# Performance work log

Measured on AMD Instinct MI355X. Metric: run time of the kernel, lower is better.

Reference implementation:

```python
import jax, jax.numpy as jnp
import numpy as np

D_MODEL = 256
N_LAYER = 16
VOCAB = 24
D_INNER = 512
D_STATE = 16
D_CONV = 4
DT_RANK = 16
B = 2
L = 2048
EPS = 1e-5


def setup_inputs() -> dict:
    key = jax.random.key(0)
    ks = jax.random.split(key, 10)
    f = lambda k, shape, s=0.02: jax.random.normal(k, shape, dtype=jnp.float32) * s
    # S4D-real style A init: A_log = log(1..d_state), broadcast over channels/layers
    a_log = jnp.tile(jnp.log(jnp.arange(1, D_STATE + 1, dtype=jnp.float32)), (N_LAYER, D_INNER, 1))
    return {
        'input_ids': jax.random.randint(ks[0], (B, L), 0, VOCAB),
        'embedding': f(ks[1], (VOCAB, D_MODEL)),
        'in_proj_w': f(ks[2], (N_LAYER, 2 * D_INNER, D_MODEL)),
        'conv_w': f(ks[3], (N_LAYER, D_INNER, D_CONV), 0.1),
        'conv_b': jnp.zeros((N_LAYER, D_INNER), dtype=jnp.float32),
        'x_proj_w': f(ks[4], (N_LAYER, DT_RANK + 2 * D_STATE, D_INNER)),
        'dt_proj_w': f(ks[5], (N_LAYER, D_INNER, DT_RANK), 0.1),
        'dt_proj_b': jnp.full((N_LAYER, D_INNER), -4.6, dtype=jnp.float32),  # softplus(-4.6) ~ 0.01 = dt_init floor
        'A_log': a_log,
        'D': jnp.ones((N_LAYER, D_INNER), dtype=jnp.float32),
        'out_proj_w': f(ks[6], (N_LAYER, D_MODEL, D_INNER), 0.005),
        'norm_w': jnp.ones((N_LAYER, D_MODEL), dtype=jnp.float32),
        'norm_f_w': jnp.ones((D_MODEL,), dtype=jnp.float32),
        'lm_head_w': f(ks[7], (20, D_MODEL)),
    }


def _rmsnorm(x, w, eps=EPS):
    return x * jax.lax.rsqrt(jnp.mean(x * x, axis=-1, keepdims=True) + eps) * w


def _selective_scan(dA, dBx, C):
    # dA, dBx: (B, L, d_inner, d_state); C: (B, L, d_state)
    # h_t = dA_t * h_{t-1} + dBx_t  (parallel associative scan over L)
    def comb(left, right):
        a_l, b_l = left
        a_r, b_r = right
        return a_l * a_r, a_r * b_l + b_r
    _, hs = jax.lax.associative_scan(comb, (dA, dBx), axis=1)
    return jnp.einsum('blds,bls->bld', hs, C)


def _mamba(h, in_w, cw, cb, xw, dtw, dtb, a_log, d_skip, ow):
    # h: (B, L, d_model)
    xz = jnp.einsum('bld,ed->ble', h, in_w)            # (B, L, 2*d_inner)
    x, z = jnp.split(xz, 2, axis=-1)
    # depthwise causal conv1d over L
    xt = jnp.transpose(x, (0, 2, 1))                   # (B, d_inner, L)
    xc = jax.lax.conv_general_dilated(
        xt, cw[:, None, :], window_strides=(1,), padding=[(D_CONV - 1, 0)],
        feature_group_count=D_INNER)
    x = jax.nn.silu(jnp.transpose(xc, (0, 2, 1)) + cb)  # (B, L, d_inner)
    dbc = jnp.einsum('bld,ed->ble', x, xw)             # (B, L, dt_rank+2*d_state)
    dt, Bm, Cm = jnp.split(dbc, [DT_RANK, DT_RANK + D_STATE], axis=-1)
    dt = jax.nn.softplus(jnp.einsum('blr,dr->bld', dt, dtw) + dtb)  # (B, L, d_inner)
    A = -jnp.exp(a_log)                                # (d_inner, d_state)
    dA = jnp.exp(dt[..., None] * A)                    # (B, L, d_inner, d_state)
    dBx = dt[..., None] * Bm[:, :, None, :] * x[..., None]
    y = _selective_scan(dA, dBx, Cm) + d_skip * x
    y = y * jax.nn.silu(z)
    return jnp.einsum('bld,ed->ble', y, ow)


def reference(input_ids, embedding, in_proj_w, conv_w, conv_b, x_proj_w,
              dt_proj_w, dt_proj_b, A_log, D, out_proj_w, norm_w, norm_f_w,
              lm_head_w):
    h = embedding[input_ids]                           # (B, L, d_model)
    residual = None
    for i in range(N_LAYER):
        residual = h + residual if residual is not None else h
        hn = _rmsnorm(residual, norm_w[i])
        h = _mamba(hn, in_proj_w[i], conv_w[i], conv_b[i], x_proj_w[i],
                   dt_proj_w[i], dt_proj_b[i], A_log[i], D[i], out_proj_w[i])
    residual = h + residual
    h = _rmsnorm(residual, norm_f_w)
    return jnp.einsum('bld,vd->blv', h, lm_head_w)     # (B, L, 20)
```

## Files before the change

### kernel.cpp

```cpp
#include <hip/hip_runtime.h>
#include <hip/hip_bf16.h>

#define D_MODEL 256
#define N_LAYER 16
#define VOCAB 24
#define D_INNER 512
#define D_STATE 16
#define D_CONV 4
#define DT_RANK 16
#define BATCH 2
#define SEQ 2048
#define NTOK (BATCH*SEQ)
#define EPS 1e-5f
#define NC 128
#define CL (SEQ/NC)
#define NSC (BATCH*D_INNER*D_STATE)
#define WCVT_BLOCKS 26112

typedef __hip_bfloat16 bf16;
typedef __attribute__((ext_vector_type(8))) short short8;
typedef __attribute__((ext_vector_type(4))) float f32x4;

__device__ __forceinline__ float silu(float v) { return v / (1.f + __expf(-v)); }
__device__ __forceinline__ float bf2f(bf16 v) { return __bfloat162float(v); }
__device__ __forceinline__ float bfs2f(short s) {
    return __uint_as_float(((unsigned)(unsigned short)s) << 16);
}
__device__ __forceinline__ short bfr(float x) {
    unsigned u = __float_as_uint(x);
    return (short)((u + 0x7fffu + ((u >> 16) & 1u)) >> 16);
}

__device__ __forceinline__ float dtdot(const float* __restrict__ rv,
                                       const float* __restrict__ wdt, float bias) {
    float p0 = bias, p1 = 0.f, p2 = 0.f, p3 = 0.f;
    #pragma unroll
    for (int r = 0; r < 4; r++) {
        p0 = fmaf(rv[r*4 + 0], wdt[r*4 + 0], p0);
        p1 = fmaf(rv[r*4 + 1], wdt[r*4 + 1], p1);
        p2 = fmaf(rv[r*4 + 2], wdt[r*4 + 2], p2);
        p3 = fmaf(rv[r*4 + 3], wdt[r*4 + 3], p3);
    }
    return (p0 + p1) + (p2 + p3);
}

__global__ void k_init(const float* __restrict__ in_w, const float* __restrict__ out_w,
                       const float* __restrict__ x_w, short* __restrict__ in_wb,
                       short* __restrict__ out_wb, short* __restrict__ x_wb,
                       const int* __restrict__ ids, const float* __restrict__ emb,
                       float* __restrict__ residual, float* __restrict__ nsum) {
    __shared__ float wred[4];
    if (blockIdx.x < WCVT_BLOCKS) {
        int idx = blockIdx.x * 256 + threadIdx.x;
        if (idx < 4194304) {
            in_wb[idx] = bfr(in_w[idx]);
        } else if (idx < 4194304 + 2097152) {
            int j = idx - 4194304;
            out_wb[j] = bfr(out_w[j]);
        } else {
            int j = idx - 4194304 - 2097152;
            x_wb[j] = bfr(x_w[j]);
        }
    } else {
        int tok = blockIdx.x - WCVT_BLOCKS, c = threadIdx.x;
        float v = emb[ids[tok] * D_MODEL + c];
        residual[tok * 256 + c] = v;
        float s = v * v;
        #pragma unroll
        for (int off = 32; off >= 1; off >>= 1) s += __shfl_xor(s, off);
        if ((c & 63) == 0) wred[c >> 6] = s;
        __syncthreads();
        if (c == 0) {
            float tot = wred[0] + wred[1] + wred[2] + wred[3];
            *(float4*)(nsum + (size_t)tok * 4) = make_float4(tot, 0.f, 0.f, 0.f);
        }
    }
}

__global__ __launch_bounds__(256) void k_gemm1_mfma(const float* __restrict__ Rres,
                                                    const float* __restrict__ nsum,
                                                    const float* __restrict__ nw,
                                                    const short* __restrict__ W16,
                                                    bf16* __restrict__ xh,
                                                    bf16* __restrict__ zb) {
    __shared__ short AsL[64 * 40];
    __shared__ short WsL[128 * 40];
    const int bm = blockIdx.x * 64, bn = blockIdx.y * 128;
    const int tid = threadIdx.x;
    const int wave = tid >> 6, lane = tid & 63;
    const int wm = (wave & 1) * 32, wn = (wave >> 1) * 32;
    const int quad = lane >> 4, lr = lane & 15;
    const int srow = tid >> 2, skq = (tid & 3) * 8;
    const float4 ns = *(const float4*)(nsum + (size_t)(bm + srow) * 4);
    const float scale = rsqrtf((ns.x + ns.y + ns.z + ns.w) * (1.f / 256.f) + EPS);
    f32x4 acc[2][2][2] = {};
    for (int k0 = 0; k0 < 256; k0 += 32) {
        float av[8], wv[8];
        *(float4*)&av[0] = *(const float4*)(Rres + (size_t)(bm + srow) * 256 + k0 + skq);
        *(float4*)&av[4] = *(const float4*)(Rres + (size_t)(bm + srow) * 256 + k0 + skq + 4);
        *(float4*)&wv[0] = *(const float4*)(nw + k0 + skq);
        *(float4*)&wv[4] = *(const float4*)(nw + k0 + skq + 4);
        short8 a8;
        #pragma unroll
        for (int j = 0; j < 8; j++) a8[j] = bfr(av[j] * scale * wv[j]);
        short8 w8[2];
        w8[0] = *(const short8*)(W16 + (size_t)(bn + srow) * 256 + k0 + skq);
        w8[1] = *(const short8*)(W16 + (size_t)(bn + 64 + srow) * 256 + k0 + skq);
        __syncthreads();
        *(short8*)&AsL[srow * 40 + skq] = a8;
        *(short8*)&WsL[srow * 40 + skq] = w8[0];
        *(short8*)&WsL[(64 + srow) * 40 + skq] = w8[1];
        __syncthreads();
        short8 af[2], bf[2][2];
        #pragma unroll
        for (int i = 0; i < 2; i++)
            af[i] = *(const short8*)&AsL[(wm + i * 16 + lr) * 40 + quad * 8];
        #pragma unroll
        for (int nb = 0; nb < 2; nb++)
            #pragma unroll
            for (int i = 0; i < 2; i++)
                bf[nb][i] = *(const short8*)&WsL[(nb * 64 + wn + i * 16 + lr) * 40 + quad * 8];
        #pragma unroll
        for (int nb = 0; nb < 2; nb++)
            #pragma unroll
            for (int mi = 0; mi < 2; mi++)
                #pragma unroll
                for (int ni = 0; ni < 2; ni++)
                    acc[nb][mi][ni] = __builtin_amdgcn_mfma_f32_16x16x32_bf16(
                        af[mi], bf[nb][ni], acc[nb][mi][ni], 0, 0, 0);
    }
    #pragma unroll
    for (int nb = 0; nb < 2; nb++) {
        #pragma unroll
        for (int mi = 0; mi < 2; mi++) {
            #pragma unroll
            for (int ni = 0; ni < 2; ni++) {
                int gcol = bn + nb * 64 + wn + ni * 16 + lr;
                #pragma unroll
                for (int r = 0; r < 4; r++) {
                    int grow = bm + wm + mi * 16 + quad * 4 + r;
                    float v = acc[nb][mi][ni][r];
                    if (gcol < 512) xh[(size_t)grow * 512 + gcol] = __float2bfloat16(v);
                    else            zb[(size_t)grow * 512 + gcol - 512] = __float2bfloat16(v);
                }
            }
        }
    }
}

__global__ __launch_bounds__(256) void k_gemm2_mfma(const bf16* __restrict__ Abf,
                                                    const short* __restrict__ W16,
                                                    float* __restrict__ residual,
                                                    float* __restrict__ nsum) {
    __shared__ short AsL[64 * 40];
    __shared__ short WsL[64 * 40];
    __shared__ float rsum[64][2];
    const short* A16 = (const short*)Abf;
    const int bm = blockIdx.x * 64, bn = blockIdx.y * 64;
    const int tid = threadIdx.x;
    const int wave = tid >> 6, lane = tid & 63;
    const int wm = (wave & 1) * 32, wn = (wave >> 1) * 32;
    const int quad = lane >> 4, lr = lane & 15;
    const int srow = tid >> 2, skq = (tid & 3) * 8;
    f32x4 acc[2][2] = {};
    for (int k0 = 0; k0 < 512; k0 += 32) {
        short8 a8 = *(const short8*)(A16 + (size_t)(bm + srow) * 512 + k0 + skq);
        short8 w8 = *(const short8*)(W16 + (size_t)(bn + srow) * 512 + k0 + skq);
        __syncthreads();
        *(short8*)&AsL[srow * 40 + skq] = a8;
        *(short8*)&WsL[srow * 40 + skq] = w8;
        __syncthreads();
        short8 af[2], bf[2];
        #pragma unroll
        for (int i = 0; i < 2; i++) {
            af[i] = *(const short8*)&AsL[(wm + i * 16 + lr) * 40 + quad * 8];
            bf[i] = *(const short8*)&WsL[(wn + i * 16 + lr) * 40 + quad * 8];
        }
        #pragma unroll
        for (int mi = 0; mi < 2; mi++)
            #pragma unroll
            for (int ni = 0; ni < 2; ni++)
                acc[mi][ni] = __builtin_amdgcn_mfma_f32_16x16x32_bf16(
                    af[mi], bf[ni], acc[mi][ni], 0, 0, 0);
    }
    float sq[2][4] = {};
    #pragma unroll
    for (int mi = 0; mi < 2; mi++) {
        #pragma unroll
        for (int ni = 0; ni < 2; ni++) {
            int gcol = bn + wn + ni * 16 + lr;
            #pragma unroll
            for (int r = 0; r < 4; r++) {
                int grow = bm + wm + mi * 16 + quad * 4 + r;
                size_t idx = (size_t)grow * 256 + gcol;
                float v = residual[idx] + acc[mi][ni][r];
                residual[idx] = v;
                sq[mi][r] += v * v;
            }
        }
    }
    #pragma unroll
    for (int off = 1; off < 16; off <<= 1) {
        #pragma unroll
        for (int mi = 0; mi < 2; mi++)
            #pragma unroll
            for (int r = 0; r < 4; r++)
                sq[mi][r] += __shfl_xor(sq[mi][r], off);
    }
    if (lr == 0) {
        #pragma unroll
        for (int mi = 0; mi < 2; mi++)
            #pragma unroll
            for (int r = 0; r < 4; r++)
                rsum[wm + mi * 16 + quad * 4 + r][wave >> 1] = sq[mi][r];
    }
    __syncthreads();
    if (tid < 64)
        nsum[(size_t)(bm + tid) * 4 + blockIdx.y] = rsum[tid][0] + rsum[tid][1];
}

__global__ __launch_bounds__(256) void k_cxs(const bf16* __restrict__ xh,
                                             const float* __restrict__ cw,
                                             const float* __restrict__ cb,
                                             const short* __restrict__ W16,
                                             const float* __restrict__ dtw,
                                             const float* __restrict__ dtb,
                                             const float* __restrict__ a_log,
                                             bf16* __restrict__ xb,
                                             float* __restrict__ dbc,
                                             float* __restrict__ Aprod,
                                             float* __restrict__ Hfin) {
    __shared__ short Cs[16][520];
    __shared__ float Ds[16][52];
    const int bm = blockIdx.x * 16;
    const int tid = threadIdx.x;
    const int wave = tid >> 6, lane = tid & 63;
    const int quad = lane >> 4, lr = lane & 15;
    const int wn = wave * 16;

    short8 wreg[16];
    if (wn < 48) {
        const short* wp = W16 + (size_t)(wn + lr) * 512 + quad * 8;
        #pragma unroll
        for (int k = 0; k < 16; k++) wreg[k] = *(const short8*)(wp + k * 32);
    }

    {
        const int d8 = (tid & 63) * 8;
        const int rg = (tid >> 6) * 4;
        const int lbase = (bm & 2047) + rg;
        const int gbase = bm + rg;
        float xv[7][8];
        #pragma unroll
        for (int i = 0; i < 7; i++) {
            int l = lbase - 3 + i;
            if (l >= 0) {
                short8 r8 = *(const short8*)((const short*)xh +
                               (size_t)(gbase - 3 + i) * 512 + d8);
                #pragma unroll
                for (int j = 0; j < 8; j++) xv[i][j] = bfs2f(r8[j]);
            } else {
                #pragma unroll
                for (int j = 0; j < 8; j++) xv[i][j] = 0.f;
            }
        }
        float cwv[8][4], cbv[8];
        #pragma unroll
        for (int j = 0; j < 8; j++) {
            *(float4*)&cwv[j][0] = *(const float4*)(cw + (d8 + j) * 4);
            cbv[j] = cb[d8 + j];
        }
        #pragma unroll
        for (int t = 0; t < 4; t++) {
            short8 o;
            #pragma unroll
            for (int j = 0; j < 8; j++) {
                float acc = cbv[j] + xv[t][j] * cwv[j][0] + xv[t+1][j] * cwv[j][1]
                                   + xv[t+2][j] * cwv[j][2] + xv[t+3][j] * cwv[j][3];
                o[j] = bfr(silu(acc));
            }
            *(short8*)&Cs[rg + t][d8] = o;
            *(short8*)((short*)xb + (size_t)(gbase + t) * 512 + d8) = o;
        }
    }
    __syncthreads();

    if (wn < 48) {
        f32x4 acc = {};
        #pragma unroll
        for (int k = 0; k < 16; k++) {
            short8 af = *(const short8*)&Cs[lr][k * 32 + quad * 8];
            acc = __builtin_amdgcn_mfma_f32_16x16x32_bf16(af, wreg[k], acc, 0, 0, 0);
        }
        int gcol = wn + lr;
        #pragma unroll
        for (int r = 0; r < 4; r++) {
            float v = acc[r];
            dbc[(size_t)(bm + quad * 4 + r) * 48 + gcol] = v;
            Ds[quad * 4 + r][gcol] = v;
        }
    }
    __syncthreads();

    {
        const int b = bm >> 11;
        const int c = (bm & 2047) >> 4;
        float A[2][16], h[2][16], ap[2][16], wdt[2][16], bdt[2];
        #pragma unroll
        for (int ch = 0; ch < 2; ch++) {
            int d = tid + ch * 256;
            #pragma unroll
            for (int q = 0; q < 4; q++)
                *(float4*)&wdt[ch][q*4] = *(const float4*)(dtw + d * 16 + q * 4);
            #pragma unroll
            for (int s = 0; s < 16; s++) {
                A[ch][s] = -__expf(a_log[d * 16 + s]);
                h[ch][s] = 0.f; ap[ch][s] = 1.f;
            }
            bdt[ch] = dtb[d];
        }
        for (int t = 0; t < CL; t++) {
            float dtc[16], Bc[16];
            #pragma unroll
            for (int r = 0; r < 16; r++) dtc[r] = Ds[t][r];
            #pragma unroll
            for (int s = 0; s < 16; s++) Bc[s] = Ds[t][16 + s];
            #pragma unroll
            for (int ch = 0; ch < 2; ch++) {
                int d = tid + ch * 256;
                float dtr = dtdot(dtc, wdt[ch], bdt[ch]);
                float dtv = (dtr > 20.f) ? dtr : __logf(1.f + __expf(dtr));
                float u = dtv * bfs2f(((const short*)&Cs[t][0])[d]);
                #pragma unroll
                for (int s = 0; s < 16; s++) {
                    float dA = __expf(dtv * A[ch][s]);
                    h[ch][s] = fmaf(dA, h[ch][s], u * Bc[s]);
                    ap[ch][s] *= dA;
                }
            }
        }
        #pragma unroll
        for (int ch = 0; ch < 2; ch++) {
            int d = tid + ch * 256;
            int bd = b * 512 + d;
            float* Ap = Aprod + (size_t)c * NSC + (size_t)bd * 16;
            float* Hp = Hfin  + (size_t)c * NSC + (size_t)bd * 16;
            #pragma unroll
            for (int q = 0; q < 4; q++) {
                *(float4*)(Ap + q * 4) = make_float4(ap[ch][q*4], ap[ch][q*4+1],
                                                     ap[ch][q*4+2], ap[ch][q*4+3]);
                *(float4*)(Hp + q * 4) = make_float4(h[ch][q*4], h[ch][q*4+1],
                                                     h[ch][q*4+2], h[ch][q*4+3]);
            }
        }
    }
}

__global__ __launch_bounds__(64) void k_scanB(const float* __restrict__ Aprod,
                                              float* __restrict__ Hfin) {
    int chain = blockIdx.x * 64 + threadIdx.x;
    float h = 0.f;
    for (int cg = 0; cg < NC; cg += 16) {
        float a[16], f[16];
        #pragma unroll
        for (int j = 0; j < 16; j++) {
            size_t i = (size_t)(cg + j) * NSC + chain;
            a[j] = Aprod[i];
            f[j] = Hfin[i];
        }
        #pragma unroll
        for (int j = 0; j < 16; j++) {
            size_t i = (size_t)(cg + j) * NSC + chain;
            Hfin[i] = h;
            h = fmaf(a[j], h, f[j]);
        }
    }
}

__global__ __launch_bounds__(64) void k_scanC(const bf16* __restrict__ xb,
                                              const bf16* __restrict__ zb,
                                              const float* __restrict__ dbc,
                                              const float* __restrict__ dtw,
                                              const float* __restrict__ dtb,
                                              const float* __restrict__ a_log,
                                              const float* __restrict__ Dp,
                                              const float* __restrict__ Hstart,
                                              bf16* __restrict__ yb) {
    __shared__ float DbcS[16 * 48];
    int gid = blockIdx.x * 64 + threadIdx.x;
    int bd = gid & 1023;
    int c = gid >> 10;
    int d = bd & 511, b = bd >> 9;
    int tok0 = b * SEQ + c * CL;
    {
        const float4* src = (const float4*)(dbc + (size_t)tok0 * 48);
        float4* dst = (float4*)DbcS;
        #pragma unroll
        for (int q = 0; q < 3; q++)
            dst[q * 64 + threadIdx.x] = src[q * 64 + threadIdx.x];
    }
    float A[16], h[16], wdt[16];
    const float* Hp = Hstart + (size_t)c * NSC + bd * 16;
    #pragma unroll
    for (int q = 0; q < 4; q++)
        *(float4*)&wdt[q*4] = *(const float4*)(dtw + d * 16 + q * 4);
    #pragma unroll
    for (int s = 0; s < 16; s++) {
        A[s] = -__expf(a_log[d * 16 + s]);
        h[s] = Hp[s];
    }
    float bdt = dtb[d];
    float Dv = Dp[d];
    const bf16* xp = xb + (size_t)tok0 * 512 + d;
    const bf16* zp = zb + (size_t)tok0 * 512 + d;
    bf16* yp = yb + (size_t)tok0 * 512 + d;
    __syncthreads();
    for (int t = 0; t < CL; t++) {
        float rv[48];
        #pragma unroll
        for (int q = 0; q < 12; q++)
            *(float4*)&rv[q*4] = *(const float4*)&DbcS[t * 48 + q * 4];
        float dtr = dtdot(rv, wdt, bdt);
        float dtv = (dtr > 20.f) ? dtr : __logf(1.f + __expf(dtr));
        float xv = bf2f(xp[t * 512]);
        float u = dtv * xv;
        float sum = 0.f;
        #pragma unroll
        for (int s = 0; s < 16; s++) {
            float dA = __expf(dtv * A[s]);
            h[s] = fmaf(dA, h[s], u * rv[16 + s]);
            sum = fmaf(h[s], rv[32 + s], sum);
        }
        float zv = bf2f(zp[t * 512]);
        yp[t * 512] = __float2bfloat16((sum + Dv * xv) * silu(zv));
    }
}

__global__ void k_rmshead(const float* __restrict__ residual, const float* __restrict__ w,
                          const float* __restrict__ lw, float* __restrict__ out) {
    __shared__ float wred[4];
    __shared__ float hrow[256];
    int tok = blockIdx.x, c = threadIdx.x;
    float v = residual[tok * 256 + c];
    float s = v * v;
    #pragma unroll
    for (int off = 32; off >= 1; off >>= 1) s += __shfl_xor(s, off);
    if ((c & 63) == 0) wred[c >> 6] = s;
    __syncthreads();
    float tot = wred[0] + wred[1] + wred[2] + wred[3];
    float scale = rsqrtf(tot * (1.f / 256.f) + EPS);
    hrow[c] = bfs2f(bfr(v * scale * w[c]));
    __syncthreads();
    int wave = c >> 6, lane = c & 63;
    float4 hl = *(const float4*)&hrow[lane * 4];
    #pragma unroll
    for (int j = 0; j < 5; j++) {
        int vv = wave * 5 + j;
        float4 wl = *(const float4*)(lw + (size_t)vv * 256 + lane * 4);
        float p = hl.x * wl.x + hl.y * wl.y + hl.z * wl.z + hl.w * wl.w;
        #pragma unroll
        for (int off = 32; off >= 1; off >>= 1) p += __shfl_xor(p, off);
        if (lane == 0) out[(size_t)tok * 20 + vv] = p;
    }
}

extern "C" void kernel_launch(void* const* d_in, const int* in_sizes, int n_in,
                              void* d_out, int out_size, void* d_ws, size_t ws_size,
                              hipStream_t stream) {
    const int*   ids    = (const int*)d_in[0];
    const float* emb    = (const float*)d_in[1];
    const float* in_w   = (const float*)d_in[2];
    const float* conv_w = (const float*)d_in[3];
    const float* conv_b = (const float*)d_in[4];
    const float* x_w    = (const float*)d_in[5];
    const float* dt_w   = (const float*)d_in[6];
    const float* dt_b   = (const float*)d_in[7];
    const float* a_log  = (const float*)d_in[8];
    const float* d_skip = (const float*)d_in[9];
    const float* out_w  = (const float*)d_in[10];
    const float* norm_w = (const float*)d_in[11];
    const float* norm_f = (const float*)d_in[12];
    const float* lm_w   = (const float*)d_in[13];
    float* out = (float*)d_out;

    char* ws = (char*)d_ws;
    float* residual = (float*)(ws + 0);
    bf16*  xh       = (bf16*) (ws + 6291456);
    bf16*  zb       = (bf16*) (ws + 10485760);
    bf16*  xb       = (bf16*) (ws + 14680064);
    float* dbc      = (float*)(ws + 18874368);
    float* Aprod    = (float*)(ws + 23855104);
    float* Hfin     = (float*)(ws + 32243712);
    short* in_wb    = (short*)(ws + 40632320);
    short* out_wb   = (short*)(ws + 49020928);
    short* x_wb     = (short*)(ws + 53215232);
    float* nsum     = (float*)(ws + 54001664);
    bf16*  yb       = xh;

    k_init<<<WCVT_BLOCKS + NTOK, 256, 0, stream>>>(in_w, out_w, x_w, in_wb, out_wb,
                                                   x_wb, ids, emb, residual, nsum);

    for (int i = 0; i < N_LAYER; i++) {
        dim3 g1(NTOK / 64, 1024 / 128);
        k_gemm1_mfma<<<g1, 256, 0, stream>>>(residual, nsum, norm_w + i * D_MODEL,
                                             in_wb + (size_t)i * 262144, xh, zb);
        k_cxs<<<NTOK / 16, 256, 0, stream>>>(
            xh, conv_w + (size_t)i * 512 * 4, conv_b + (size_t)i * 512,
            x_wb + (size_t)i * 24576, dt_w + (size_t)i * 512 * 16,
            dt_b + (size_t)i * 512, a_log + (size_t)i * 512 * 16,
            xb, dbc, Aprod, Hfin);
        k_scanB<<<NSC / 64, 64, 0, stream>>>(Aprod, Hfin);
        k_scanC<<<(1024 * NC) / 64, 64, 0, stream>>>(
            xb, zb, dbc, dt_w + (size_t)i * 512 * 16, dt_b + (size_t)i * 512,
            a_log + (size_t)i * 512 * 16, d_skip + (size_t)i * 512, Hfin, yb);
        dim3 g2(NTOK / 64, 256 / 64);
        k_gemm2_mfma<<<g2, 256, 0, stream>>>(yb, out_wb + (size_t)i * 131072,
                                             residual, nsum);
    }

    k_rmshead<<<NTOK, 256, 0, stream>>>(residual, norm_f, lm_w, out);
}
```

Before: 1.124 ms.

## Fuse chunked scan output pass with out_proj GEMM and residual update

Merges the scan-output kernel and the out_proj GEMM into one kernel. Each block handles one 16-token chunk: it runs the scan for all 512 channels (two channels per thread), writes y into shared memory as bf16, then runs an MFMA GEMM against the full 256x512 out_proj weight and updates the residual and the partial RMS sums. This avoids writing y to global memory, reading it back, and one launch per layer. In exchange each block reloads the whole weight matrix, parallelism drops from 2048 blocks of 64 threads to 256 blocks of 256 threads, and the GEMM runs with only 16 rows per block.

```diff
diff --git a/kernel.cpp b/kernel.cpp
--- a/kernel.cpp
+++ b/kernel.cpp
@@ -148,77 +148,6 @@
     }
 }
 
-__global__ __launch_bounds__(256) void k_gemm2_mfma(const bf16* __restrict__ Abf,
-                                                    const short* __restrict__ W16,
-                                                    float* __restrict__ residual,
-                                                    float* __restrict__ nsum) {
-    __shared__ short AsL[64 * 40];
-    __shared__ short WsL[64 * 40];
-    __shared__ float rsum[64][2];
-    const short* A16 = (const short*)Abf;
-    const int bm = blockIdx.x * 64, bn = blockIdx.y * 64;
-    const int tid = threadIdx.x;
-    const int wave = tid >> 6, lane = tid & 63;
-    const int wm = (wave & 1) * 32, wn = (wave >> 1) * 32;
-    const int quad = lane >> 4, lr = lane & 15;
-    const int srow = tid >> 2, skq = (tid & 3) * 8;
-    f32x4 acc[2][2] = {};
-    for (int k0 = 0; k0 < 512; k0 += 32) {
-        short8 a8 = *(const short8*)(A16 + (size_t)(bm + srow) * 512 + k0 + skq);
-        short8 w8 = *(const short8*)(W16 + (size_t)(bn + srow) * 512 + k0 + skq);
-        __syncthreads();
-        *(short8*)&AsL[srow * 40 + skq] = a8;
-        *(short8*)&WsL[srow * 40 + skq] = w8;
-        __syncthreads();
-        short8 af[2], bf[2];
-        #pragma unroll
-        for (int i = 0; i < 2; i++) {
-            af[i] = *(const short8*)&AsL[(wm + i * 16 + lr) * 40 + quad * 8];
-            bf[i] = *(const short8*)&WsL[(wn + i * 16 + lr) * 40 + quad * 8];
-        }
-        #pragma unroll
-        for (int mi = 0; mi < 2; mi++)
-            #pragma unroll
-            for (int ni = 0; ni < 2; ni++)
-                acc[mi][ni] = __builtin_amdgcn_mfma_f32_16x16x32_bf16(
-                    af[mi], bf[ni], acc[mi][ni], 0, 0, 0);
-    }
-    float sq[2][4] = {};
-    #pragma unroll
-    for (int mi = 0; mi < 2; mi++) {
-        #pragma unroll
-        for (int ni = 0; ni < 2; ni++) {
-            int gcol = bn + wn + ni * 16 + lr;
-            #pragma unroll
-            for (int r = 0; r < 4; r++) {
-                int grow = bm + wm + mi * 16 + quad * 4 + r;
-                size_t idx = (size_t)grow * 256 + gcol;
-                float v = residual[idx] + acc[mi][ni][r];
-                residual[idx] = v;
-                sq[mi][r] += v * v;
-            }
-        }
-    }
-    #pragma unroll
-    for (int off = 1; off < 16; off <<= 1) {
-        #pragma unroll
-        for (int mi = 0; mi < 2; mi++)
-            #pragma unroll
-            for (int r = 0; r < 4; r++)
-                sq[mi][r] += __shfl_xor(sq[mi][r], off);
-    }
-    if (lr == 0) {
-        #pragma unroll
-        for (int mi = 0; mi < 2; mi++)
-            #pragma unroll
-            for (int r = 0; r < 4; r++)
-                rsum[wm + mi * 16 + quad * 4 + r][wave >> 1] = sq[mi][r];
-    }
-    __syncthreads();
-    if (tid < 64)
-        nsum[(size_t)(bm + tid) * 4 + blockIdx.y] = rsum[tid][0] + rsum[tid][1];
-}
-
 __global__ __launch_bounds__(256) void k_cxs(const bf16* __restrict__ xh,
                                              const float* __restrict__ cw,
                                              const float* __restrict__ cb,
@@ -377,62 +306,116 @@
     }
 }
 
-__global__ __launch_bounds__(64) void k_scanC(const bf16* __restrict__ xb,
-                                              const bf16* __restrict__ zb,
-                                              const float* __restrict__ dbc,
-                                              const float* __restrict__ dtw,
-                                              const float* __restrict__ dtb,
-                                              const float* __restrict__ a_log,
-                                              const float* __restrict__ Dp,
-                                              const float* __restrict__ Hstart,
-                                              bf16* __restrict__ yb) {
+__global__ __launch_bounds__(256) void k_sg2(const bf16* __restrict__ xb,
+                                             const bf16* __restrict__ zb,
+                                             const float* __restrict__ dbc,
+                                             const float* __restrict__ dtw,
+                                             const float* __restrict__ dtb,
+                                             const float* __restrict__ a_log,
+                                             const float* __restrict__ Dp,
+                                             const float* __restrict__ Hstart,
+                                             const short* __restrict__ W16,
+                                             float* __restrict__ residual,
+                                             float* __restrict__ nsum) {
+    __shared__ short Ys[16][520];
     __shared__ float DbcS[16 * 48];
-    int gid = blockIdx.x * 64 + threadIdx.x;
-    int bd = gid & 1023;
-    int c = gid >> 10;
-    int d = bd & 511, b = bd >> 9;
-    int tok0 = b * SEQ + c * CL;
-    {
-        const float4* src = (const float4*)(dbc + (size_t)tok0 * 48);
-        float4* dst = (float4*)DbcS;
-        #pragma unroll
-        for (int q = 0; q < 3; q++)
-            dst[q * 64 + threadIdx.x] = src[q * 64 + threadIdx.x];
-    }
-    float A[16], h[16], wdt[16];
-    const float* Hp = Hstart + (size_t)c * NSC + bd * 16;
-    #pragma unroll
-    for (int q = 0; q < 4; q++)
-        *(float4*)&wdt[q*4] = *(const float4*)(dtw + d * 16 + q * 4);
-    #pragma unroll
-    for (int s = 0; s < 16; s++) {
-        A[s] = -__expf(a_log[d * 16 + s]);
-        h[s] = Hp[s];
-    }
-    float bdt = dtb[d];
-    float Dv = Dp[d];
-    const bf16* xp = xb + (size_t)tok0 * 512 + d;
-    const bf16* zp = zb + (size_t)tok0 * 512 + d;
-    bf16* yp = yb + (size_t)tok0 * 512 + d;
+    __shared__ short Ws[256 * 40];
+    const int bm = blockIdx.x * 16;
+    const int tid = threadIdx.x;
+    const int b = bm >> 11;
+    const int c = (bm & 2047) >> 4;
+
+    if (tid < 192)
+        ((float4*)DbcS)[tid] = ((const float4*)(dbc + (size_t)bm * 48))[tid];
+
+    float A[2][16], h[2][16], wdt[2][16], bdt[2], Dv[2];
+    #pragma unroll
+    for (int ch = 0; ch < 2; ch++) {
+        int d = tid + ch * 256;
+        int bd = b * 512 + d;
+        const float* Hp = Hstart + (size_t)c * NSC + (size_t)bd * 16;
+        #pragma unroll
+        for (int q = 0; q < 4; q++)
+            *(float4*)&wdt[ch][q*4] = *(const float4*)(dtw + d * 16 + q * 4);
+        #pragma unroll
+        for (int s = 0; s < 16; s++) {
+            A[ch][s] = -__expf(a_log[d * 16 + s]);
+            h[ch][s] = Hp[s];
+        }
+        bdt[ch] = dtb[d];
+        Dv[ch] = Dp[d];
+    }
     __syncthreads();
+
     for (int t = 0; t < CL; t++) {
         float rv[48];
         #pragma unroll
         for (int q = 0; q < 12; q++)
             *(float4*)&rv[q*4] = *(const float4*)&DbcS[t * 48 + q * 4];
-        float dtr = dtdot(rv, wdt, bdt);
-        float dtv = (dtr > 20.f) ? dtr : __logf(1.f + __expf(dtr));
-        float xv = bf2f(xp[t * 512]);
-        float u = dtv * xv;
-        float sum = 0.f;
-        #pragma unroll
-        for (int s = 0; s < 16; s++) {
-            float dA = __expf(dtv * A[s]);
-            h[s] = fmaf(dA, h[s], u * rv[16 + s]);
-            sum = fmaf(h[s], rv[32 + s], sum);
-        }
-        float zv = bf2f(zp[t * 512]);
-        yp[t * 512] = __float2bfloat16((sum + Dv * xv) * silu(zv));
+        #pragma unroll
+        for (int ch = 0; ch < 2; ch++) {
+            int d = tid + ch * 256;
+            float dtr = dtdot(rv, wdt[ch], bdt[ch]);
+            float dtv = (dtr > 20.f) ? dtr : __logf(1.f + __expf(dtr));
+            float xv = bf2f(xb[(size_t)(bm + t) * 512 + d]);
+            float u = dtv * xv;
+            float sum = 0.f;
+            #pragma unroll
+            for (int s = 0; s < 16; s++) {
+                float dA = __expf(dtv * A[ch][s]);
+                h[ch][s] = fmaf(dA, h[ch][s], u * rv[16 + s]);
+                sum = fmaf(h[ch][s], rv[32 + s], sum);
+            }
+            float zv = bf2f(zb[(size_t)(bm + t) * 512 + d]);
+            Ys[t][d] = bfr((sum + Dv[ch] * xv) * silu(zv));
+        }
+    }
+    __syncthreads();
+
+    const int wave = tid >> 6, lane = tid & 63;
+    const int quad = lane >> 4, lr = lane & 15;
+    const int wn = wave * 64;
+    f32x4 acc[4] = {};
+    for (int k0 = 0; k0 < 512; k0 += 32) {
+        short8 w8[4];
+        #pragma unroll
+        for (int j = 0; j < 4; j++)
+            w8[j] = *(const short8*)(W16 + (size_t)tid * 512 + k0 + j * 8);
+        __syncthreads();
+        #pragma unroll
+        for (int j = 0; j < 4; j++)
+            *(short8*)&Ws[tid * 40 + j * 8] = w8[j];
+        __syncthreads();
+        short8 af = *(const short8*)&Ys[lr][k0 + quad * 8];
+        #pragma unroll
+        for (int ni = 0; ni < 4; ni++) {
+            short8 bfv = *(const short8*)&Ws[(wn + ni * 16 + lr) * 40 + quad * 8];
+            acc[ni] = __builtin_amdgcn_mfma_f32_16x16x32_bf16(af, bfv, acc[ni], 0, 0, 0);
+        }
+    }
+    float sq[4] = {0.f, 0.f, 0.f, 0.f};
+    #pragma unroll
+    for (int ni = 0; ni < 4; ni++) {
+        int gcol = wn + ni * 16 + lr;
+        #pragma unroll
+        for (int r = 0; r < 4; r++) {
+            int grow = bm + quad * 4 + r;
+            size_t idx = (size_t)grow * 256 + gcol;
+            float v = residual[idx] + acc[ni][r];
+            residual[idx] = v;
+            sq[r] += v * v;
+        }
+    }
+    #pragma unroll
+    for (int off = 1; off < 16; off <<= 1) {
+        #pragma unroll
+        for (int r = 0; r < 4; r++)
+            sq[r] += __shfl_xor(sq[r], off);
+    }
+    if (lr == 0) {
+        #pragma unroll
+        for (int r = 0; r < 4; r++)
+            nsum[(size_t)(bm + quad * 4 + r) * 4 + wave] = sq[r];
     }
 }
 
@@ -495,7 +478,6 @@
     short* out_wb   = (short*)(ws + 49020928);
     short* x_wb     = (short*)(ws + 53215232);
     float* nsum     = (float*)(ws + 54001664);
-    bf16*  yb       = xh;
 
     k_init<<<WCVT_BLOCKS + NTOK, 256, 0, stream>>>(in_w, out_w, x_w, in_wb, out_wb,
                                                    x_wb, ids, emb, residual, nsum);
@@ -510,12 +492,10 @@
             dt_b + (size_t)i * 512, a_log + (size_t)i * 512 * 16,
             xb, dbc, Aprod, Hfin);
         k_scanB<<<NSC / 64, 64, 0, stream>>>(Aprod, Hfin);
-        k_scanC<<<(1024 * NC) / 64, 64, 0, stream>>>(
+        k_sg2<<<NTOK / 16, 256, 0, stream>>>(
             xb, zb, dbc, dt_w + (size_t)i * 512 * 16, dt_b + (size_t)i * 512,
-            a_log + (size_t)i * 512 * 16, d_skip + (size_t)i * 512, Hfin, yb);
-        dim3 g2(NTOK / 64, 256 / 64);
-        k_gemm2_mfma<<<g2, 256, 0, stream>>>(yb, out_wb + (size_t)i * 131072,
-                                             residual, nsum);
+            a_log + (size_t)i * 512 * 16, d_skip + (size_t)i * 512, Hfin,
+            out_wb + (size_t)i * 131072, residual, nsum);
     }
 
     k_rmshead<<<NTOK, 256, 0, stream>>>(residual, norm_f, lm_w, out);
```

Measured after the change: 1.187 ms. +5.6%, slower.
